# Optimization experiments

Hardware: AMD Instinct MI355X
Metric: run time of the kernel (lower is better)

## Reference

```python
import jax, jax.numpy as jnp
import numpy as np

# Module constants (match init_kwargs)
E = 8           # num_experts
K = 2           # num_experts_per_tok
BLOCK = 16      # BLOCK_SIZE hardcoded in module
NORM_TOPK = True


def setup_inputs() -> dict:
    key = jax.random.key(0)
    k0, k1, k2, k3 = jax.random.split(key, 4)
    B, S, H = 2, 2048, 768
    F = 4 * H  # ffn_hidden_size
    x = jax.random.normal(k0, (B, S, H), dtype=jnp.float32)
    router_w = jax.random.normal(k1, (E, H), dtype=jnp.float32) * 0.02
    # kaiming-uniform-ish scale for w1/w2
    w1 = jax.random.uniform(k2, (H, E * F), dtype=jnp.float32, minval=-1.0, maxval=1.0) * float(1.0 / np.sqrt(H))
    w2 = jax.random.uniform(k3, (E * F, H), dtype=jnp.float32, minval=-1.0, maxval=1.0) * float(1.0 / np.sqrt(E * F))
    return {"x": x, "router_w": router_w, "w1": w1, "w2": w2}


def _moe_forward(x, router_w, w1, w2):
    B, S, H = x.shape
    T = B * S
    x_flat = x.reshape(T, H)

    # Router
    router_logits = x_flat @ router_w.T                      # [T, E]
    rw = jax.nn.softmax(router_logits.astype(jnp.float32), axis=-1)
    top_w, sel = jax.lax.top_k(rw, K)                        # [T, K]
    if NORM_TOPK:
        top_w = top_w / top_w.sum(axis=-1, keepdims=True)
    top_w = top_w.astype(x.dtype)  # NOTE: computed but NOT applied in combine (faithful to source)

    # Block-padding multiplicities (faithful to source's duplicate-last-token padding bug):
    # assignments are sorted stably by expert; the LAST assignment of each expert's
    # group is duplicated pad_e = (-count_e) % BLOCK times and then scatter-added.
    sel_flat = sel.reshape(-1)                               # [T*K], token-major stable order
    flat_idx = jnp.arange(T * K, dtype=jnp.int32)
    counts = jax.ops.segment_sum(jnp.ones((T * K,), jnp.int32), sel_flat, num_segments=E)
    pad = (-counts) % BLOCK                                  # [E]
    last_idx = jax.ops.segment_max(flat_idx, sel_flat, num_segments=E)  # [E]
    mult = 1 + jnp.where(flat_idx == last_idx[sel_flat], pad[sel_flat], 0)  # [T*K]

    # Combine coefficients coef[t, e] = multiplicity of (token t, expert e) assignment
    token_ids = flat_idx // K
    coef = jnp.zeros((T, E), dtype=x.dtype).at[token_ids, sel_flat].add(mult.astype(x.dtype))

    # Expert FFNs: y1 = gelu(x @ W1_e) @ W2_e, combined with coef (NOT routing weights)
    F = w1.shape[1] // E
    w1e = w1.reshape(H, E, F)
    w2e = w2.reshape(E, F, H)
    out = jnp.zeros((T, H), dtype=x.dtype)
    for e in range(E):  # small fixed loop over experts
        h = jax.nn.gelu(x_flat @ w1e[:, e, :], approximate=False)  # [T, F]
        out = out + coef[:, e:e + 1] * (h @ w2e[e])                # [T, H]

    return out.reshape(B, S, H), router_logits


def reference(x, router_w, w1, w2):
    return _moe_forward(x, router_w, w1, w2)
```

## Files before the change

### kernel.cpp

```cpp
#include <hip/hip_runtime.h>
#include <math.h>

#define T_TOK 4096
#define H_DIM 768
#define E_NUM 8
#define F_DIM 3072
#define EF_DIM 24576
#define BK 64
#define SEG_MAX 9216
#define MAX_TILES 72
#define TILE_SH (128 * BK)

#define OFF_CNT      0
#define OFF_LAST     8
#define OFF_NT      40
#define OFF_TOTAL   41
#define OFF_SCHED_E 48
#define OFF_SCHED_G 120

#define WS_SEL   768
#define WS_TOK   33536
#define WS_COEF  70400
#define WS_XG    107264ull
#define WS_HG    14263040ull
#define WS_WT    70886144ull

typedef __attribute__((ext_vector_type(8))) short short8;
typedef __attribute__((ext_vector_type(4))) float float4v;

__device__ __forceinline__ short f2b(float f) {
  union { float f; unsigned u; } v; v.f = f;
  unsigned r = v.u + 0x7FFFu + ((v.u >> 16) & 1u);
  return (short)(r >> 16);
}
__device__ __forceinline__ float b2f(short s) {
  union { unsigned u; float f; } v; v.u = ((unsigned)(unsigned short)s) << 16;
  return v.f;
}
__device__ __forceinline__ float gelu_fast(float v) {
  const float z = 1.5957691216f * fmaf(0.044715f * v * v, v, v);
  return v / (1.0f + __expf(-z));
}
__device__ __forceinline__ void gl_lds16(const void* g, void* l) {
  __builtin_amdgcn_global_load_lds(
      (const __attribute__((address_space(1))) void*)g,
      (__attribute__((address_space(3))) void*)l, 16, 0, 0);
}

__global__ __launch_bounds__(256) void router_k(const float* __restrict__ x,
                                                const float* __restrict__ rw,
                                                float* __restrict__ logits_out,
                                                int* __restrict__ sel) {
  __shared__ float rws[E_NUM * H_DIM];
  for (int i = threadIdx.x; i < E_NUM * H_DIM; i += 256) rws[i] = rw[i];
  __syncthreads();
  const int wid = threadIdx.x >> 6, lane = threadIdx.x & 63;
  const int t = blockIdx.x * 4 + wid;
  const float* xr = x + (size_t)t * H_DIM;
  double acc[E_NUM];
#pragma unroll
  for (int e = 0; e < E_NUM; ++e) acc[e] = 0.0;
  for (int i = 0; i < H_DIM / 64; ++i) {
    const int h = lane + 64 * i;
    const float xv = xr[h];
#pragma unroll
    for (int e = 0; e < E_NUM; ++e) acc[e] += (double)xv * (double)rws[e * H_DIM + h];
  }
#pragma unroll
  for (int e = 0; e < E_NUM; ++e)
    for (int off = 32; off; off >>= 1) acc[e] += __shfl_down(acc[e], off);
  if (lane == 0) {
    float lg[E_NUM];
#pragma unroll
    for (int e = 0; e < E_NUM; ++e) { lg[e] = (float)acc[e]; logits_out[t * E_NUM + e] = lg[e]; }
    int e0 = 0;
    for (int e = 1; e < E_NUM; ++e) if (lg[e] > lg[e0]) e0 = e;
    int e1 = -1;
    for (int e = 0; e < E_NUM; ++e) {
      if (e == e0) continue;
      if (e1 < 0 || lg[e] > lg[e1]) e1 = e;
    }
    sel[t * 2 + 0] = e0;
    sel[t * 2 + 1] = e1;
  }
}

__global__ __launch_bounds__(1024) void hist_k(const int* __restrict__ sel,
                                               int* __restrict__ meta) {
  const int e = blockIdx.x;
  const int tid = threadIdx.x, lane = tid & 63, wid = tid >> 6;
  __shared__ int wcnt[16], wlast[16];
  int c = 0, lmax = 0;
#pragma unroll
  for (int it = 0; it < 8; ++it) {
    const int a = it * 1024 + tid;
    const unsigned long long mask = __ballot(sel[a] == e);
    if (lane == 0 && mask) {
      c += (int)__popcll(mask);
      const int hi = 63 - (int)__clzll((long long)mask);
      const int cand = a + hi + 1;
      lmax = lmax > cand ? lmax : cand;
    }
  }
  if (lane == 0) { wcnt[wid] = c; wlast[wid] = lmax; }
  __syncthreads();
  if (tid == 0) {
    int C = 0, L = 0;
    for (int w = 0; w < 16; ++w) { C += wcnt[w]; L = L > wlast[w] ? L : wlast[w]; }
    meta[OFF_CNT + e] = C;
    meta[OFF_LAST + e] = L;
  }
}

__global__ __launch_bounds__(1024) void scatter_k(const int* __restrict__ sel,
                                                  int* __restrict__ meta,
                                                  int* __restrict__ tok,
                                                  float* __restrict__ coefv) {
  const int e = blockIdx.x;
  const int tid = threadIdx.x, lane = tid & 63, wid = tid >> 6;
  __shared__ int wv[16];

  int cnt[E_NUM];
#pragma unroll
  for (int i = 0; i < E_NUM; ++i) cnt[i] = meta[OFF_CNT + i];
  int seg = 0;
  for (int i = 0; i < e; ++i) seg += (cnt[i] + 127) & ~127;
  const int c = cnt[e];
  const int ru = (c + 127) & ~127;
  const int pad = (16 - (c & 15)) & 15;
  const int laste = meta[OFF_LAST + e];
  const float lastcoef = (float)(1 + pad);

  for (int p = c + tid; p < ru; p += 1024) { tok[seg + p] = -1; coefv[seg + p] = 0.0f; }
  if (e == E_NUM - 1) {
    const int total = seg + ru;
    for (int p = total + tid; p < SEG_MAX; p += 1024) { tok[p] = -1; coefv[p] = 0.0f; }
  }

  if (e == 0) {
    int nt = 0, s2 = 0;
    for (int i = 0; i < E_NUM; ++i) {
      const int rui = (cnt[i] + 127) & ~127;
      for (int m = 0; m < rui; m += 128) {
        if (nt == tid) { meta[OFF_SCHED_E + nt] = i; meta[OFF_SCHED_G + nt] = s2 + m; }
        ++nt;
      }
      s2 += rui;
    }
    if (tid >= nt && tid < MAX_TILES) { meta[OFF_SCHED_E + tid] = -1; meta[OFF_SCHED_G + tid] = 0; }
    if (tid == 0) { meta[OFF_NT] = nt; meta[OFF_TOTAL] = s2; }
  }

  int running = 0;
#pragma unroll
  for (int it = 0; it < 8; ++it) {
    const int a = it * 1024 + tid;
    const bool f = (sel[a] == e);
    const unsigned long long mask = __ballot(f);
    if (lane == 0) wv[wid] = (int)__popcll(mask);
    __syncthreads();
    int pre = 0, tot = 0;
#pragma unroll
    for (int w = 0; w < 16; ++w) { const int v = wv[w]; pre += (w < wid) ? v : 0; tot += v; }
    if (f) {
      const int rank = (int)__popcll(mask & ((1ull << lane) - 1ull));
      const int g = seg + running + pre + rank;
      tok[g] = a;
      coefv[g] = (laste == a + 1) ? lastcoef : 1.0f;
    }
    running += tot;
    __syncthreads();
  }
}

__global__ __launch_bounds__(256) void pos_k(const int* __restrict__ tok, int* __restrict__ pos) {
  const int g = blockIdx.x * 256 + threadIdx.x;
  const int a = tok[g];
  if (a >= 0) pos[a] = g;
}

__global__ __launch_bounds__(256) void gather_x_k(const float* __restrict__ x,
                                                  const int* __restrict__ tok,
                                                  short* __restrict__ xg) {
  const int u = blockIdx.x * 256 + threadIdx.x;
  const int g = u / 96;
  const int c = (u - g * 96) * 8;
  const int a = tok[g];
  short8 v = {0, 0, 0, 0, 0, 0, 0, 0};
  if (a >= 0) {
    const float* src = x + (size_t)(a >> 1) * H_DIM + c;
    float4v f0 = *(const float4v*)src;
    float4v f1 = *(const float4v*)(src + 4);
    v[0] = f2b(f0[0]); v[1] = f2b(f0[1]); v[2] = f2b(f0[2]); v[3] = f2b(f0[3]);
    v[4] = f2b(f1[0]); v[5] = f2b(f1[1]); v[6] = f2b(f1[2]); v[7] = f2b(f1[3]);
  }
  *(short8*)&xg[(size_t)g * H_DIM + c] = v;
}

__global__ __launch_bounds__(256) void conv_w1_k(const float* __restrict__ w1, short* __restrict__ w1f) {
  __shared__ float tile[64][65];
  const int n0 = blockIdx.x * 64;
  const int h0 = blockIdx.y * 64;
  const int tid = threadIdx.x;
  const int rr = tid >> 4;
  const int cc = (tid & 15) * 4;
#pragma unroll
  for (int p = 0; p < 4; ++p) {
    const int r = p * 16 + rr;
    float4v f = *(const float4v*)(w1 + (size_t)(h0 + r) * EF_DIM + n0 + cc);
    tile[r][cc] = f[0]; tile[r][cc + 1] = f[1]; tile[r][cc + 2] = f[2]; tile[r][cc + 3] = f[3];
  }
  __syncthreads();
#pragma unroll
  for (int p = 0; p < 2; ++p) {
    const int item = p * 256 + tid;
    const int nl = item >> 3;
    const int u8 = item & 7;
    short8 v;
#pragma unroll
    for (int j = 0; j < 8; ++j) v[j] = f2b(tile[u8 * 8 + j][nl]);
    const size_t dst = (size_t)(((n0 + nl) >> 4) * (H_DIM / 64) + (h0 >> 6)) * 1024 +
                       u8 * 128 + (nl & 15) * 8;
    *(short8*)(w1f + dst) = v;
  }
}

__global__ __launch_bounds__(256) void conv_w2_k(const float* __restrict__ w2, short* __restrict__ w2f) {
  __shared__ float tile[64][65];
  const int k0 = blockIdx.x * 64;
  const int h0 = blockIdx.y * 64;
  const int e = k0 / F_DIM;
  const int f0 = k0 - e * F_DIM;
  const int tid = threadIdx.x;
  const int rr = tid >> 4;
  const int cc = (tid & 15) * 4;
#pragma unroll
  for (int p = 0; p < 4; ++p) {
    const int r = p * 16 + rr;
    float4v f = *(const float4v*)(w2 + (size_t)(k0 + r) * H_DIM + h0 + cc);
    tile[r][cc] = f[0]; tile[r][cc + 1] = f[1]; tile[r][cc + 2] = f[2]; tile[r][cc + 3] = f[3];
  }
  __syncthreads();
#pragma unroll
  for (int p = 0; p < 2; ++p) {
    const int item = p * 256 + tid;
    const int nl = item >> 3;
    const int u8 = item & 7;
    short8 v;
#pragma unroll
    for (int j = 0; j < 8; ++j) v[j] = f2b(tile[u8 * 8 + j][nl]);
    const size_t dst = (size_t)e * ((H_DIM / 16) * (F_DIM / 64) * 1024) +
                       (size_t)(((h0 + nl) >> 4) * (F_DIM / 64) + (f0 >> 6)) * 1024 +
                       u8 * 128 + (nl & 15) * 8;
    *(short8*)(w2f + dst) = v;
  }
}


#define G_ITER(T, CB, BCUR, BNXT, NT, BSTR, NJ)                                        \
  {                                                                                    \
    const int nb_ = TILE_SH - (CB);                                                    \
    if ((T) + 1 < (NT)) {                                                              \
      const int k0n_ = ((T) + 1) * BK;                                                 \
      _Pragma("unroll")                                                                \
      for (int i = 0; i < 4; ++i) gl_lds16(agp[i] + k0n_, &As[nb_ + loff[i]]);         \
    }                                                                                  \
    const int tn_ = ((T) + 1 < (NT)) ? (T) + 1 : (T);                                  \
    _Pragma("unroll")                                                                  \
    for (int s = 0; s < 2; ++s)                                                        \
      _Pragma("unroll")                                                                \
      for (int j = 0; j < (NJ); ++j)                                                   \
        BNXT[s][j] = *(const short8*)(bb + (size_t)j * (BSTR) + tn_ * 1024 + s * 512); \
    short8 a_frag[2][4];                                                               \
    _Pragma("unroll")                                                                  \
    for (int s = 0; s < 2; ++s) {                                                      \
      const int csw_ = ((s * 4 + q) ^ rsw) * 8;                                        \
      _Pragma("unroll")                                                                \
      for (int i = 0; i < 4; ++i)                                                      \
        a_frag[s][i] = *(const short8*)&As[(CB) + (mw + 16 * i + lrow) * BK + csw_];   \
    }                                                                                  \
    _Pragma("unroll")                                                                  \
    for (int s = 0; s < 2; ++s)                                                        \
      _Pragma("unroll")                                                                \
      for (int i = 0; i < 4; ++i)                                                      \
        _Pragma("unroll")                                                              \
        for (int j = 0; j < (NJ); ++j)                                                 \
          acc[i][j] = __builtin_amdgcn_mfma_f32_16x16x32_bf16(a_frag[s][i], BCUR[s][j],\
                                                              acc[i][j], 0, 0, 0);     \
    asm volatile("s_waitcnt vmcnt(0) lgkmcnt(0)" ::: "memory");                        \
    __builtin_amdgcn_s_barrier();                                                      \
  }

__global__ __launch_bounds__(256, 2) void gemm1_k(const short* __restrict__ xg,
                                                  const short* __restrict__ w1f,
                                                  const int* __restrict__ meta,
                                                  short* __restrict__ hg) {
  const unsigned hwL = blockIdx.x;
  const unsigned logical = (hwL & 7u) * 216u + (hwL >> 3);
  const int slot = (int)(logical / 24u);
  const int n0 = (int)(logical % 24u) * 128;
  if (slot >= meta[OFF_NT]) return;
  const int e = meta[OFF_SCHED_E + slot];
  const int gbase = meta[OFF_SCHED_G + slot];

  __shared__ short As[2 * TILE_SH];

  const int tid = threadIdx.x;
  const int w = tid >> 6, l = tid & 63;
  const int mw = (w & 1) * 64, nw = (w >> 1) * 64;
  const int lrow = l & 15, q = l >> 4;
  const int srow = l >> 3;
  const int schunk = (l & 7) ^ srow;

  const short* agp[4];
  int loff[4];
#pragma unroll
  for (int i = 0; i < 4; ++i) {
    const int r = i * 32 + w * 8 + srow;
    agp[i] = xg + (size_t)(gbase + r) * H_DIM + schunk * 8;
    loff[i] = (i * 32 + w * 8) * BK + l * 8;
  }
  const int rsw = lrow & 7;
  const short* bb = w1f + (size_t)((e * F_DIM + n0 + nw) >> 4) * ((H_DIM / 64) * 1024) +
                    q * 128 + lrow * 8;

  float4v acc[4][4] = {};
  short8 bX[2][4], bY[2][4];

#pragma unroll
  for (int i = 0; i < 4; ++i) gl_lds16(agp[i], &As[loff[i]]);
#pragma unroll
  for (int s = 0; s < 2; ++s)
#pragma unroll
    for (int j = 0; j < 4; ++j)
      bX[s][j] = *(const short8*)(bb + (size_t)j * ((H_DIM / 64) * 1024) + s * 512);
  asm volatile("s_waitcnt vmcnt(0)" ::: "memory");
  __builtin_amdgcn_s_barrier();

  const int NT = H_DIM / BK;
  for (int t = 0; t < NT; t += 2) {
    G_ITER(t, 0, bX, bY, NT, (H_DIM / 64) * 1024, 4)
    G_ITER(t + 1, TILE_SH, bY, bX, NT, (H_DIM / 64) * 1024, 4)
  }

  short* Ep = As;
#pragma unroll
  for (int i = 0; i < 4; ++i)
#pragma unroll
    for (int j = 0; j < 4; ++j)
#pragma unroll
      for (int r = 0; r < 4; ++r) {
        const int row = mw + 16 * i + q * 4 + r;
        const int col = nw + 16 * j + lrow;
        Ep[row * 128 + (col ^ ((row & 7) << 4))] = f2b(gelu_fast(acc[i][j][r]));
      }
  __syncthreads();
#pragma unroll
  for (int p = 0; p < 8; ++p) {
    const int item = p * 256 + tid;
    const int row = item >> 4;
    const int cc8 = (item & 15) * 8;
    const short8 v = *(const short8*)&Ep[row * 128 + (cc8 ^ ((row & 7) << 4))];
    *(short8*)&hg[(size_t)(gbase + row) * F_DIM + n0 + cc8] = v;
  }
}

__global__ __launch_bounds__(256, 2) void gemm2_k(const short* __restrict__ hg,
                                                  const short* __restrict__ w2f,
                                                  const int* __restrict__ meta,
                                                  short* __restrict__ tmp) {
  const unsigned hwL = blockIdx.x;
  const unsigned xcd = hwL & 7u;
  const unsigned l2 = hwL >> 3;
  const int slot = (int)(xcd * 9u + l2 / 12u);
  const int n0 = (int)(l2 % 12u) * 64;
  if (slot >= meta[OFF_NT]) return;
  const int e = meta[OFF_SCHED_E + slot];
  const int gbase = meta[OFF_SCHED_G + slot];

  __shared__ short As[2 * TILE_SH];

  const int tid = threadIdx.x;
  const int w = tid >> 6, l = tid & 63;
  const int mw = (w & 1) * 64, nw = (w >> 1) * 32;
  const int lrow = l & 15, q = l >> 4;
  const int srow = l >> 3;
  const int schunk = (l & 7) ^ srow;

  const short* agp[4];
  int loff[4];
#pragma unroll
  for (int i = 0; i < 4; ++i) {
    const int r = i * 32 + w * 8 + srow;
    agp[i] = hg + (size_t)(gbase + r) * F_DIM + schunk * 8;
    loff[i] = (i * 32 + w * 8) * BK + l * 8;
  }
  const int rsw = lrow & 7;
  const short* bb = w2f + (size_t)e * ((H_DIM / 16) * (F_DIM / 64) * 1024) +
                    (size_t)((n0 + nw) >> 4) * ((F_DIM / 64) * 1024) +
                    q * 128 + lrow * 8;

  float4v acc[4][2] = {};
  short8 bX[2][2], bY[2][2];

#pragma unroll
  for (int i = 0; i < 4; ++i) gl_lds16(agp[i], &As[loff[i]]);
#pragma unroll
  for (int s = 0; s < 2; ++s)
#pragma unroll
    for (int j = 0; j < 2; ++j)
      bX[s][j] = *(const short8*)(bb + (size_t)j * ((F_DIM / 64) * 1024) + s * 512);
  asm volatile("s_waitcnt vmcnt(0)" ::: "memory");
  __builtin_amdgcn_s_barrier();

  const int NT = F_DIM / BK;
  for (int t = 0; t < NT; t += 2) {
    G_ITER(t, 0, bX, bY, NT, (F_DIM / 64) * 1024, 2)
    G_ITER(t + 1, TILE_SH, bY, bX, NT, (F_DIM / 64) * 1024, 2)
  }

  short* Ep = As;
#pragma unroll
  for (int i = 0; i < 4; ++i)
#pragma unroll
    for (int j = 0; j < 2; ++j)
#pragma unroll
      for (int r = 0; r < 4; ++r) {
        const int row = mw + 16 * i + q * 4 + r;
        const int col = nw + 16 * j + lrow;
        Ep[row * 128 + (col ^ ((row & 7) << 4))] = f2b(acc[i][j][r]);
      }
  __syncthreads();
#pragma unroll
  for (int p = 0; p < 4; ++p) {
    const int item = p * 256 + tid;
    const int row = item >> 3;
    const int cc8 = (item & 7) * 8;
    const short8 v = *(const short8*)&Ep[row * 128 + (cc8 ^ ((row & 7) << 4))];
    *(short8*)&tmp[(size_t)(gbase + row) * H_DIM + n0 + cc8] = v;
  }
}

__global__ __launch_bounds__(256) void combine_k(const short* __restrict__ tmp,
                                                 const int* __restrict__ pos,
                                                 const float* __restrict__ coefv,
                                                 float* __restrict__ out) {
  const int u = blockIdx.x * 256 + threadIdx.x;
  const int t = u / 96;
  const int c = (u - t * 96) * 8;
  const int g0 = pos[t * 2 + 0];
  const int g1 = pos[t * 2 + 1];
  const float c0 = coefv[g0];
  const float c1 = coefv[g1];
  const short8 v0 = *(const short8*)&tmp[(size_t)g0 * H_DIM + c];
  const short8 v1 = *(const short8*)&tmp[(size_t)g1 * H_DIM + c];
  float r[8];
#pragma unroll
  for (int j = 0; j < 8; ++j) r[j] = c0 * b2f(v0[j]) + c1 * b2f(v1[j]);
  float4v* dst = (float4v*)&out[(size_t)t * H_DIM + c];
  dst[0] = (float4v){r[0], r[1], r[2], r[3]};
  dst[1] = (float4v){r[4], r[5], r[6], r[7]};
}

extern "C" void kernel_launch(void* const* d_in, const int* in_sizes, int n_in,
                              void* d_out, int out_size, void* d_ws, size_t ws_size,
                              hipStream_t stream) {
  const float* x  = (const float*)d_in[0];
  const float* rw = (const float*)d_in[1];
  const float* w1 = (const float*)d_in[2];
  const float* w2 = (const float*)d_in[3];
  float* out = (float*)d_out;
  float* logits = out + (size_t)T_TOK * H_DIM;

  char* ws = (char*)d_ws;
  int*   meta  = (int*)ws;
  int*   sel   = (int*)(ws + WS_SEL);
  int*   tok   = (int*)(ws + WS_TOK);
  float* coefv = (float*)(ws + WS_COEF);
  short* xg    = (short*)(ws + WS_XG);
  short* hg    = (short*)(ws + WS_HG);
  short* wt    = (short*)(ws + WS_WT);

  conv_w1_k<<<dim3(EF_DIM / 64, H_DIM / 64), 256, 0, stream>>>(w1, wt);
  router_k<<<T_TOK / 4, 256, 0, stream>>>(x, rw, logits, sel);
  hist_k<<<E_NUM, 1024, 0, stream>>>(sel, meta);
  scatter_k<<<E_NUM, 1024, 0, stream>>>(sel, meta, tok, coefv);
  pos_k<<<SEG_MAX / 256, 256, 0, stream>>>(tok, sel);
  gather_x_k<<<(SEG_MAX * (H_DIM / 8)) / 256, 256, 0, stream>>>(x, tok, xg);
  gemm1_k<<<24 * MAX_TILES, 256, 0, stream>>>(xg, wt, meta, hg);
  conv_w2_k<<<dim3(EF_DIM / 64, H_DIM / 64), 256, 0, stream>>>(w2, wt);
  gemm2_k<<<12 * MAX_TILES, 256, 0, stream>>>(hg, wt, meta, xg);
  combine_k<<<(T_TOK * 96) / 256, 256, 0, stream>>>(xg, sel, coefv, out);
}
```

Measured before the change: 350.9 us.

## Pre-swizzle activations into MFMA fragment layout and load A directly to registers

Result: slower. 419.0 us (+19.4%).

```diff
diff --git a/kernel.cpp b/kernel.cpp
--- a/kernel.cpp
+++ b/kernel.cpp
@@ -6,10 +6,8 @@
 #define E_NUM 8
 #define F_DIM 3072
 #define EF_DIM 24576
-#define BK 64
 #define SEG_MAX 9216
 #define MAX_TILES 72
-#define TILE_SH (128 * BK)
 
 #define OFF_CNT      0
 #define OFF_LAST     8
@@ -40,11 +38,6 @@
 __device__ __forceinline__ float gelu_fast(float v) {
   const float z = 1.5957691216f * fmaf(0.044715f * v * v, v, v);
   return v / (1.0f + __expf(-z));
-}
-__device__ __forceinline__ void gl_lds16(const void* g, void* l) {
-  __builtin_amdgcn_global_load_lds(
-      (const __attribute__((address_space(1))) void*)g,
-      (__attribute__((address_space(3))) void*)l, 16, 0, 0);
 }
 
 __global__ __launch_bounds__(256) void router_k(const float* __restrict__ x,
@@ -181,7 +174,7 @@
 
 __global__ __launch_bounds__(256) void gather_x_k(const float* __restrict__ x,
                                                   const int* __restrict__ tok,
-                                                  short* __restrict__ xg) {
+                                                  short* __restrict__ xgf) {
   const int u = blockIdx.x * 256 + threadIdx.x;
   const int g = u / 96;
   const int c = (u - g * 96) * 8;
@@ -194,7 +187,8 @@
     v[0] = f2b(f0[0]); v[1] = f2b(f0[1]); v[2] = f2b(f0[2]); v[3] = f2b(f0[3]);
     v[4] = f2b(f1[0]); v[5] = f2b(f1[1]); v[6] = f2b(f1[2]); v[7] = f2b(f1[3]);
   }
-  *(short8*)&xg[(size_t)g * H_DIM + c] = v;
+  const size_t dst = (size_t)((g >> 4) * 12 + (c >> 6)) * 1024 + ((c >> 3) & 7) * 128 + (g & 15) * 8;
+  *(short8*)&xgf[dst] = v;
 }
 
 __global__ __launch_bounds__(256) void conv_w1_k(const float* __restrict__ w1, short* __restrict__ w1f) {
@@ -257,44 +251,33 @@
 }
 
 
-#define G_ITER(T, CB, BCUR, BNXT, NT, BSTR, NJ)                                        \
+#define GG_ITER(T, ACUR, ANXT, BCUR, BNXT, NT, ASTR, BSTR, NJ)                         \
   {                                                                                    \
-    const int nb_ = TILE_SH - (CB);                                                    \
-    if ((T) + 1 < (NT)) {                                                              \
-      const int k0n_ = ((T) + 1) * BK;                                                 \
+    const int tn_ = ((T) + 1 < (NT)) ? (T) + 1 : (T);                                  \
+    _Pragma("unroll")                                                                  \
+    for (int s = 0; s < 2; ++s)                                                        \
       _Pragma("unroll")                                                                \
-      for (int i = 0; i < 4; ++i) gl_lds16(agp[i] + k0n_, &As[nb_ + loff[i]]);         \
-    }                                                                                  \
-    const int tn_ = ((T) + 1 < (NT)) ? (T) + 1 : (T);                                  \
+      for (int i = 0; i < 4; ++i)                                                      \
+        ANXT[s][i] = *(const short8*)(ab + (size_t)i * (ASTR) + tn_ * 1024 + s * 512); \
     _Pragma("unroll")                                                                  \
     for (int s = 0; s < 2; ++s)                                                        \
       _Pragma("unroll")                                                                \
       for (int j = 0; j < (NJ); ++j)                                                   \
         BNXT[s][j] = *(const short8*)(bb + (size_t)j * (BSTR) + tn_ * 1024 + s * 512); \
-    short8 a_frag[2][4];                                                               \
-    _Pragma("unroll")                                                                  \
-    for (int s = 0; s < 2; ++s) {                                                      \
-      const int csw_ = ((s * 4 + q) ^ rsw) * 8;                                        \
-      _Pragma("unroll")                                                                \
-      for (int i = 0; i < 4; ++i)                                                      \
-        a_frag[s][i] = *(const short8*)&As[(CB) + (mw + 16 * i + lrow) * BK + csw_];   \
-    }                                                                                  \
     _Pragma("unroll")                                                                  \
     for (int s = 0; s < 2; ++s)                                                        \
       _Pragma("unroll")                                                                \
       for (int i = 0; i < 4; ++i)                                                      \
         _Pragma("unroll")                                                              \
         for (int j = 0; j < (NJ); ++j)                                                 \
-          acc[i][j] = __builtin_amdgcn_mfma_f32_16x16x32_bf16(a_frag[s][i], BCUR[s][j],\
+          acc[i][j] = __builtin_amdgcn_mfma_f32_16x16x32_bf16(ACUR[s][i], BCUR[s][j],  \
                                                               acc[i][j], 0, 0, 0);     \
-    asm volatile("s_waitcnt vmcnt(0) lgkmcnt(0)" ::: "memory");                        \
-    __builtin_amdgcn_s_barrier();                                                      \
-  }
-
-__global__ __launch_bounds__(256, 2) void gemm1_k(const short* __restrict__ xg,
+  }
+
+__global__ __launch_bounds__(256, 2) void gemm1_k(const short* __restrict__ xgf,
                                                   const short* __restrict__ w1f,
                                                   const int* __restrict__ meta,
-                                                  short* __restrict__ hg) {
+                                                  short* __restrict__ hgf) {
   const unsigned hwL = blockIdx.x;
   const unsigned logical = (hwL & 7u) * 216u + (hwL >> 3);
   const int slot = (int)(logical / 24u);
@@ -303,47 +286,35 @@
   const int e = meta[OFF_SCHED_E + slot];
   const int gbase = meta[OFF_SCHED_G + slot];
 
-  __shared__ short As[2 * TILE_SH];
+  __shared__ short Ep[128 * 128];
 
   const int tid = threadIdx.x;
   const int w = tid >> 6, l = tid & 63;
   const int mw = (w & 1) * 64, nw = (w >> 1) * 64;
   const int lrow = l & 15, q = l >> 4;
-  const int srow = l >> 3;
-  const int schunk = (l & 7) ^ srow;
-
-  const short* agp[4];
-  int loff[4];
-#pragma unroll
-  for (int i = 0; i < 4; ++i) {
-    const int r = i * 32 + w * 8 + srow;
-    agp[i] = xg + (size_t)(gbase + r) * H_DIM + schunk * 8;
-    loff[i] = (i * 32 + w * 8) * BK + l * 8;
-  }
-  const int rsw = lrow & 7;
-  const short* bb = w1f + (size_t)((e * F_DIM + n0 + nw) >> 4) * ((H_DIM / 64) * 1024) +
-                    q * 128 + lrow * 8;
+
+  const short* ab = xgf + (size_t)((gbase + mw) >> 4) * (12 * 1024) + l * 8;
+  const short* bb = w1f + (size_t)((e * F_DIM + n0 + nw) >> 4) * (12 * 1024) + l * 8;
 
   float4v acc[4][4] = {};
-  short8 bX[2][4], bY[2][4];
-
-#pragma unroll
-  for (int i = 0; i < 4; ++i) gl_lds16(agp[i], &As[loff[i]]);
+  short8 aX[2][4], aY[2][4], bX[2][4], bY[2][4];
+
 #pragma unroll
   for (int s = 0; s < 2; ++s)
 #pragma unroll
+    for (int i = 0; i < 4; ++i)
+      aX[s][i] = *(const short8*)(ab + (size_t)i * 12288 + s * 512);
+#pragma unroll
+  for (int s = 0; s < 2; ++s)
+#pragma unroll
     for (int j = 0; j < 4; ++j)
-      bX[s][j] = *(const short8*)(bb + (size_t)j * ((H_DIM / 64) * 1024) + s * 512);
-  asm volatile("s_waitcnt vmcnt(0)" ::: "memory");
-  __builtin_amdgcn_s_barrier();
-
-  const int NT = H_DIM / BK;
-  for (int t = 0; t < NT; t += 2) {
-    G_ITER(t, 0, bX, bY, NT, (H_DIM / 64) * 1024, 4)
-    G_ITER(t + 1, TILE_SH, bY, bX, NT, (H_DIM / 64) * 1024, 4)
-  }
-
-  short* Ep = As;
+      bX[s][j] = *(const short8*)(bb + (size_t)j * 12288 + s * 512);
+
+  for (int t = 0; t < 12; t += 2) {
+    GG_ITER(t, aX, aY, bX, bY, 12, 12288, 12288, 4)
+    GG_ITER(t + 1, aY, aX, bY, bX, 12, 12288, 12288, 4)
+  }
+
 #pragma unroll
   for (int i = 0; i < 4; ++i)
 #pragma unroll
@@ -361,11 +332,14 @@
     const int row = item >> 4;
     const int cc8 = (item & 15) * 8;
     const short8 v = *(const short8*)&Ep[row * 128 + (cc8 ^ ((row & 7) << 4))];
-    *(short8*)&hg[(size_t)(gbase + row) * F_DIM + n0 + cc8] = v;
-  }
-}
-
-__global__ __launch_bounds__(256, 2) void gemm2_k(const short* __restrict__ hg,
+    const int f = n0 + cc8;
+    const size_t dst = (size_t)((gbase + row) >> 4) * (48 * 1024) + (f >> 6) * 1024 +
+                       ((f >> 3) & 7) * 128 + (row & 15) * 8;
+    *(short8*)&hgf[dst] = v;
+  }
+}
+
+__global__ __launch_bounds__(256, 2) void gemm2_k(const short* __restrict__ hgf,
                                                   const short* __restrict__ w2f,
                                                   const int* __restrict__ meta,
                                                   short* __restrict__ tmp) {
@@ -378,48 +352,36 @@
   const int e = meta[OFF_SCHED_E + slot];
   const int gbase = meta[OFF_SCHED_G + slot];
 
-  __shared__ short As[2 * TILE_SH];
+  __shared__ short Ep[128 * 128];
 
   const int tid = threadIdx.x;
   const int w = tid >> 6, l = tid & 63;
   const int mw = (w & 1) * 64, nw = (w >> 1) * 32;
   const int lrow = l & 15, q = l >> 4;
-  const int srow = l >> 3;
-  const int schunk = (l & 7) ^ srow;
-
-  const short* agp[4];
-  int loff[4];
-#pragma unroll
-  for (int i = 0; i < 4; ++i) {
-    const int r = i * 32 + w * 8 + srow;
-    agp[i] = hg + (size_t)(gbase + r) * F_DIM + schunk * 8;
-    loff[i] = (i * 32 + w * 8) * BK + l * 8;
-  }
-  const int rsw = lrow & 7;
+
+  const short* ab = hgf + (size_t)((gbase + mw) >> 4) * (48 * 1024) + l * 8;
   const short* bb = w2f + (size_t)e * ((H_DIM / 16) * (F_DIM / 64) * 1024) +
-                    (size_t)((n0 + nw) >> 4) * ((F_DIM / 64) * 1024) +
-                    q * 128 + lrow * 8;
+                    (size_t)((n0 + nw) >> 4) * (48 * 1024) + l * 8;
 
   float4v acc[4][2] = {};
-  short8 bX[2][2], bY[2][2];
-
-#pragma unroll
-  for (int i = 0; i < 4; ++i) gl_lds16(agp[i], &As[loff[i]]);
+  short8 aX[2][4], aY[2][4], bX[2][2], bY[2][2];
+
 #pragma unroll
   for (int s = 0; s < 2; ++s)
 #pragma unroll
+    for (int i = 0; i < 4; ++i)
+      aX[s][i] = *(const short8*)(ab + (size_t)i * 49152 + s * 512);
+#pragma unroll
+  for (int s = 0; s < 2; ++s)
+#pragma unroll
     for (int j = 0; j < 2; ++j)
-      bX[s][j] = *(const short8*)(bb + (size_t)j * ((F_DIM / 64) * 1024) + s * 512);
-  asm volatile("s_waitcnt vmcnt(0)" ::: "memory");
-  __builtin_amdgcn_s_barrier();
-
-  const int NT = F_DIM / BK;
-  for (int t = 0; t < NT; t += 2) {
-    G_ITER(t, 0, bX, bY, NT, (F_DIM / 64) * 1024, 2)
-    G_ITER(t + 1, TILE_SH, bY, bX, NT, (F_DIM / 64) * 1024, 2)
-  }
-
-  short* Ep = As;
+      bX[s][j] = *(const short8*)(bb + (size_t)j * 49152 + s * 512);
+
+  for (int t = 0; t < 48; t += 2) {
+    GG_ITER(t, aX, aY, bX, bY, 48, 49152, 49152, 2)
+    GG_ITER(t + 1, aY, aX, bY, bX, 48, 49152, 49152, 2)
+  }
+
 #pragma unroll
   for (int i = 0; i < 4; ++i)
 #pragma unroll
```
